# Kernel tuning notes

Hardware: AMD Instinct MI355X
Metric: run time of the kernel (lower is better)

## Reference

```python
import jax, jax.numpy as jnp
import numpy as np

N_WIRES = 4
BATCH, SEQ, EMBED, FFN = 8, 512, 512, 2048


def setup_inputs() -> dict:
    key = jax.random.key(0)
    k_x, k_w1, k_w2 = jax.random.split(key, 3)
    x = jax.random.normal(k_x, (BATCH, SEQ, EMBED), dtype=jnp.float32)
    # Linear params (torch Linear: y = x @ W^T + b; we store pre-transposed)
    W1 = jax.random.normal(k_w1, (EMBED, FFN), dtype=jnp.float32) / np.sqrt(EMBED)
    b1 = jnp.zeros((FFN,), dtype=jnp.float32)
    W2 = jax.random.normal(k_w2, (FFN, EMBED), dtype=jnp.float32) / np.sqrt(FFN)
    b2 = jnp.zeros((EMBED,), dtype=jnp.float32)
    return {"x": x, "W1": W1, "b1": b1, "W2": W2, "b2": b2}


def reference(x, W1, b1, W2, b2):
    b, s, d = x.shape
    flat = x.reshape(b * s, d)                      # [n, d], n = b*s
    # Quantum kernel: circuit RY(x_i) then RY(-y_i) per wire on |0..0>;
    # |0..0> amplitude = prod_i cos((x_i - y_i)/2); only first n_wires feats used
    # (reset_states(1) + states.view(-1)[0] selects batch row 0 of the reshape).
    f = flat[:, :N_WIRES]                           # [n, nw]
    half_diff = (f[:, None, :] - f[None, :, :]) * 0.5   # [n, n, nw]
    gram = jnp.abs(jnp.prod(jnp.cos(half_diff), axis=-1))  # [n, n]
    out = gram @ flat                               # [n, d]
    h = jax.nn.relu(out @ W1 + b1)                  # [n, ffn]  (dropout = eval identity)
    y = h @ W2 + b2                                 # [n, d]
    return y.reshape(b, s, d)
```

## Files before the change

kernel.cpp:

```cpp
#include <hip/hip_runtime.h>
#include <hip/hip_bf16.h>
#include <stdint.h>

using bf = __bf16;
typedef __attribute__((ext_vector_type(8))) __bf16 bf16x8;
typedef __attribute__((ext_vector_type(4))) float f32x4;
typedef __attribute__((ext_vector_type(4))) int i32x4;

#define M_TOT 4096
#define D_EMB 512
#define F_FFN 2048

__device__ __forceinline__ void gload_lds16(const void* g, void* l) {
  __builtin_amdgcn_global_load_lds(
      (const __attribute__((address_space(1))) uint32_t*)g,
      (__attribute__((address_space(3))) uint32_t*)l, 16, 0, 0);
}

__device__ __forceinline__ int swz128(int row, int b) {
  return row * 128 + (b ^ ((row & 7) << 4));
}
__device__ __forceinline__ bf16x8 ldf128(const char* base, int row, int b) {
  return *(const bf16x8*)(base + swz128(row, b));
}
__device__ __forceinline__ i32x4 ldf128i(const char* base, int row, int b) {
  return *(const i32x4*)(base + swz128(row, b));
}
template <int CHUNKS>
__device__ __forceinline__ void stage_rows4(const void* gsrc, size_t ld_bytes, char* lbase,
                                            int wave, int lane) {
  const int rsub = lane >> 3, csub = lane & 7;
  const int sc = csub ^ rsub;
#pragma unroll
  for (int i = 0; i < CHUNKS / 4; ++i) {
    int chunk = wave + i * 4;
    int row = chunk * 8 + rsub;
    gload_lds16((const char*)gsrc + (size_t)row * ld_bytes + sc * 16, lbase + chunk * 1024);
  }
}
__device__ __forceinline__ int quant_i8(float x, float s) {
  float v = x * s;
  v = fminf(127.f, fmaxf(-127.f, v));
  return (int)rintf(v);
}

#define NB_SGEN 1024
#define NT_FT   2048
#define NT_W1   1024
#define NT_W2   1024

__global__ __launch_bounds__(256) void k_prep(const float* __restrict__ x,
                                              const float* __restrict__ W1,
                                              const float* __restrict__ W2,
                                              int8_t* __restrict__ fi8, bf* __restrict__ w1T,
                                              bf* __restrict__ w2T, int8_t* __restrict__ S) {
  __shared__ __align__(16) char smem[32768];
  const int bid = blockIdx.x, tid = threadIdx.x;

  if (bid < NB_SGEN) {
    char* phiL = smem;
    char* st = smem + 16384;
    const int e = bid & 7, idx = bid >> 3;
    const int jt = e * 4 + (idx & 3);
    const int mt = idx >> 2;
    const int m0 = mt * 128;
    const int j0 = jt * 128;
    {
      int g = (tid < 128) ? (m0 + tid) : (j0 + tid - 128);
      float c[4], s[4];
#pragma unroll
      for (int k = 0; k < 4; ++k) {
        float f = x[(size_t)g * D_EMB + k] * 0.5f;
        sincosf(f, &s[k], &c[k]);
      }
      bf* row = (bf*)(phiL + tid * 64);
#pragma unroll
      for (int m = 0; m < 16; ++m) {
        float p = 1.0f;
#pragma unroll
        for (int k = 0; k < 4; ++k) p *= ((m >> k) & 1) ? s[k] : c[k];
        row[m] = (bf)p;
      }
#pragma unroll
      for (int m = 16; m < 32; ++m) row[m] = (bf)0.0f;
    }
    __syncthreads();

    const int wave = tid >> 6, lane = tid & 63;
    const int lr = lane & 15, lg = lane >> 4;
    const bf16x8 a0 = *(const bf16x8*)(phiL + (wave * 32 + lr) * 64 + lg * 16);
    const bf16x8 a1 = *(const bf16x8*)(phiL + (wave * 32 + 16 + lr) * 64 + lg * 16);

    const int mb0 = wave * 32 + lg * 4;
    const int key = (lr & 7) << 4;
#pragma unroll
    for (int jf = 0; jf < 8; ++jf) {
      bf16x8 b = *(const bf16x8*)(phiL + (128 + jf * 16 + lr) * 64 + lg * 16);
      f32x4 s0 = __builtin_amdgcn_mfma_f32_16x16x32_bf16(a0, b, f32x4{0.f, 0.f, 0.f, 0.f}, 0, 0, 0);
      f32x4 s1 = __builtin_amdgcn_mfma_f32_16x16x32_bf16(a1, b, f32x4{0.f, 0.f, 0.f, 0.f}, 0, 0, 0);
      uint32_t w0 = 0, w1 = 0;
#pragma unroll
      for (int r = 0; r < 4; ++r) {
        uint32_t q0 = (uint32_t)min(127, (int)rintf(fabsf(s0[r]) * 127.f));
        uint32_t q1 = (uint32_t)min(127, (int)rintf(fabsf(s1[r]) * 127.f));
        w0 |= q0 << (8 * r);
        w1 |= q1 << (8 * r);
      }
      int jrow = jf * 16 + lr;
      *(uint32_t*)(st + jrow * 128 + (mb0 ^ key)) = w0;
      *(uint32_t*)(st + jrow * 128 + ((mb0 + 16) ^ key)) = w1;
    }
    __syncthreads();
#pragma unroll
    for (int i = 0; i < 4; ++i) {
      int idx2 = tid + i * 256;
      int jrow = idx2 >> 3, seg = idx2 & 7;
      i32x4 v = *(const i32x4*)(st + jrow * 128 + ((seg * 16) ^ ((jrow & 7) << 4)));
      *(i32x4*)(S + (size_t)(j0 + jrow) * M_TOT + m0 + seg * 16) = v;
    }
    return;
  }

  float(*tile)[33] = (float(*)[33])smem;
  const int tx = tid & 31, ty = tid >> 5;
  if (bid < NB_SGEN + NT_FT) {
    int b2 = bid - NB_SGEN;
    int c0 = (b2 % (D_EMB / 32)) * 32, r0 = (b2 / (D_EMB / 32)) * 32;
#pragma unroll
    for (int i = 0; i < 32; i += 8)
      tile[ty + i][tx] = x[(size_t)(r0 + ty + i) * D_EMB + c0 + tx];
    __syncthreads();
#pragma unroll
    for (int i = 0; i < 32; i += 8)
      fi8[(size_t)(c0 + ty + i) * M_TOT + r0 + tx] = (int8_t)quant_i8(tile[tx][ty + i], 15.875f);
  } else if (bid < NB_SGEN + NT_FT + NT_W1) {
    int b2 = bid - NB_SGEN - NT_FT;
    int c0 = (b2 % (F_FFN / 32)) * 32, r0 = (b2 / (F_FFN / 32)) * 32;
#pragma unroll
    for (int i = 0; i < 32; i += 8)
      tile[ty + i][tx] = W1[(size_t)(r0 + ty + i) * F_FFN + c0 + tx];
    __syncthreads();
#pragma unroll
    for (int i = 0; i < 32; i += 8)
      w1T[(size_t)(c0 + ty + i) * D_EMB + r0 + tx] = (bf)tile[tx][ty + i];
  } else {
    int b2 = bid - NB_SGEN - NT_FT - NT_W1;
    int c0 = (b2 % (D_EMB / 32)) * 32, r0 = (b2 / (D_EMB / 32)) * 32;
#pragma unroll
    for (int i = 0; i < 32; i += 8)
      tile[ty + i][tx] = W2[(size_t)(r0 + ty + i) * D_EMB + c0 + tx];
    __syncthreads();
#pragma unroll
    for (int i = 0; i < 32; i += 8)
      w2T[(size_t)(c0 + ty + i) * F_FFN + r0 + tx] = (bf)tile[tx][ty + i];
  }
}

template <int OUTMODE>
__global__ __launch_bounds__(256, 3) void k_g64(const bf* __restrict__ A, const bf* __restrict__ BT,
                                                const float* __restrict__ bias, void* __restrict__ out,
                                                int N, int K) {
  constexpr int BUF = 16384;
  __shared__ __align__(16) char sm[3 * BUF];

  const int tid = threadIdx.x;
  const int wave = tid >> 6, lane = tid & 63;
  const int lr = lane & 15, lg = lane >> 4;
  const int wm = wave & 1, wn = wave >> 1;

  const int lin = blockIdx.x;
  const int e = lin & 7, jj = lin >> 3;
  const int bm = e * 8 + (jj & 7), bn = jj >> 3;
  const int m0 = bm * 64, n0 = bn * 64;

  f32x4 acc[2][2];
#pragma unroll
  for (int i = 0; i < 2; ++i)
#pragma unroll
    for (int f = 0; f < 2; ++f) acc[i][f] = f32x4{0.f, 0.f, 0.f, 0.f};

  const size_t ldb = (size_t)K * 2;
  stage_rows4<8>(A + (size_t)m0 * K, ldb, sm, wave, lane);
  stage_rows4<8>(BT + (size_t)n0 * K, ldb, sm + 8192, wave, lane);
  stage_rows4<8>(A + (size_t)m0 * K + 64, ldb, sm + BUF, wave, lane);
  stage_rows4<8>(BT + (size_t)n0 * K + 64, ldb, sm + BUF + 8192, wave, lane);

  const int NT = K / 64;
  for (int t = 0; t < NT; ++t) {
    char* aTc = sm + (t % 3) * BUF;
    char* bTc = aTc + 8192;
    if (t + 1 < NT) asm volatile("s_waitcnt vmcnt(4)" ::: "memory");
    else            asm volatile("s_waitcnt vmcnt(0)" ::: "memory");
    __builtin_amdgcn_s_barrier();

    if (t + 2 < NT) {
      char* aTn = sm + ((t + 2) % 3) * BUF;
      stage_rows4<8>(A + (size_t)m0 * K + (t + 2) * 64, ldb, aTn, wave, lane);
      stage_rows4<8>(BT + (size_t)n0 * K + (t + 2) * 64, ldb, aTn + 8192, wave, lane);
    }
#pragma unroll
    for (int ksl = 0; ksl < 2; ++ksl) {
      bf16x8 a[2], b[2];
#pragma unroll
      for (int i = 0; i < 2; ++i) a[i] = ldf128(aTc, wm * 32 + i * 16 + lr, (ksl * 32 + lg * 8) * 2);
#pragma unroll
      for (int f = 0; f < 2; ++f) b[f] = ldf128(bTc, wn * 32 + f * 16 + lr, (ksl * 32 + lg * 8) * 2);
#pragma unroll
      for (int i = 0; i < 2; ++i)
#pragma unroll
        for (int f = 0; f < 2; ++f)
          acc[i][f] = __builtin_amdgcn_mfma_f32_16x16x32_bf16(a[i], b[f], acc[i][f], 0, 0, 0);
    }
  }

#pragma unroll
  for (int f = 0; f < 2; ++f) {
    int n = n0 + wn * 32 + f * 16 + lr;
    float bv = bias[n];
#pragma unroll
    for (int i = 0; i < 2; ++i)
#pragma unroll
      for (int r = 0; r < 4; ++r) {
        int m = m0 + wm * 32 + i * 16 + lg * 4 + r;
        float v = acc[i][f][r] + bv;
        if (OUTMODE == 1) {
          v = v > 0.f ? v : 0.f;
          ((bf*)out)[(size_t)m * N + n] = (bf)v;
        } else {
          ((float*)out)[(size_t)m * N + n] = v;
        }
      }
  }
}

__global__ __launch_bounds__(256, 3) void k_gi64(const int8_t* __restrict__ S,
                                                 const int8_t* __restrict__ FT,
                                                 bf* __restrict__ outb) {
  constexpr int BUF = 16384;
  __shared__ __align__(16) char sm[3 * BUF];

  const int tid = threadIdx.x;
  const int wave = tid >> 6, lane = tid & 63;
  const int lr = lane & 15, lg = lane >> 4;
  const int wm = wave & 1, wn = wave >> 1;

  const int lin = blockIdx.x;
  const int e = lin & 7, jj = lin >> 3;
  const int bm = e * 8 + (jj & 7), bn = jj >> 3;
  const int m0 = bm * 64, n0 = bn * 64;

  i32x4 acc[2][2];
#pragma unroll
  for (int i = 0; i < 2; ++i)
#pragma unroll
    for (int f = 0; f < 2; ++f) acc[i][f] = i32x4{0, 0, 0, 0};

  stage_rows4<8>(S + (size_t)m0 * M_TOT, M_TOT, sm, wave, lane);
  stage_rows4<8>(FT + (size_t)n0 * M_TOT, M_TOT, sm + 8192, wave, lane);
  stage_rows4<8>(S + (size_t)m0 * M_TOT + 128, M_TOT, sm + BUF, wave, lane);
  stage_rows4<8>(FT + (size_t)n0 * M_TOT + 128, M_TOT, sm + BUF + 8192, wave, lane);

  constexpr int NT = M_TOT / 128;
  for (int t = 0; t < NT; ++t) {
    char* aTc = sm + (t % 3) * BUF;
    char* bTc = aTc + 8192;
    if (t + 1 < NT) asm volatile("s_waitcnt vmcnt(4)" ::: "memory");
    else            asm volatile("s_waitcnt vmcnt(0)" ::: "memory");
    __builtin_amdgcn_s_barrier();

    if (t + 2 < NT) {
      char* aTn = sm + ((t + 2) % 3) * BUF;
      stage_rows4<8>(S + (size_t)m0 * M_TOT + (t + 2) * 128, M_TOT, aTn, wave, lane);
      stage_rows4<8>(FT + (size_t)n0 * M_TOT + (t + 2) * 128, M_TOT, aTn + 8192, wave, lane);
    }
#pragma unroll
    for (int ksub = 0; ksub < 2; ++ksub) {
      i32x4 a[2], b[2];
#pragma unroll
      for (int i = 0; i < 2; ++i) a[i] = ldf128i(aTc, wm * 32 + i * 16 + lr, ksub * 64 + lg * 16);
#pragma unroll
      for (int f = 0; f < 2; ++f) b[f] = ldf128i(bTc, wn * 32 + f * 16 + lr, ksub * 64 + lg * 16);
#pragma unroll
      for (int i = 0; i < 2; ++i)
#pragma unroll
        for (int f = 0; f < 2; ++f)
          acc[i][f] = __builtin_amdgcn_mfma_i32_16x16x64_i8(a[i], b[f], acc[i][f], 0, 0, 0);
    }
  }

  constexpr float SCALE = 8.0f / 16129.0f;
#pragma unroll
  for (int f = 0; f < 2; ++f) {
    int n = n0 + wn * 32 + f * 16 + lr;
#pragma unroll
    for (int i = 0; i < 2; ++i)
#pragma unroll
      for (int r = 0; r < 4; ++r) {
        int m = m0 + wm * 32 + i * 16 + lg * 4 + r;
        outb[(size_t)m * D_EMB + n] = (bf)((float)acc[i][f][r] * SCALE);
      }
  }
}

constexpr size_t OFF_FI8  = 0;
constexpr size_t OFF_OUTB = OFF_FI8 + (size_t)D_EMB * M_TOT;
constexpr size_t OFF_W1T  = OFF_OUTB + (size_t)M_TOT * D_EMB * 2;
constexpr size_t OFF_W2T  = OFF_W1T + (size_t)F_FFN * D_EMB * 2;
constexpr size_t OFF_S    = OFF_W2T + (size_t)D_EMB * F_FFN * 2;
constexpr size_t OFF_HB   = OFF_S;

extern "C" void kernel_launch(void* const* d_in, const int* in_sizes, int n_in,
                              void* d_out, int out_size, void* d_ws, size_t ws_size,
                              hipStream_t stream) {
  const float* x  = (const float*)d_in[0];
  const float* W1 = (const float*)d_in[1];
  const float* b1 = (const float*)d_in[2];
  const float* W2 = (const float*)d_in[3];
  const float* b2 = (const float*)d_in[4];
  float* y = (float*)d_out;
  char* ws = (char*)d_ws;

  int8_t* fi8 = (int8_t*)(ws + OFF_FI8);
  bf* outb    = (bf*)(ws + OFF_OUTB);
  bf* w1T     = (bf*)(ws + OFF_W1T);
  bf* w2T     = (bf*)(ws + OFF_W2T);
  int8_t* S   = (int8_t*)(ws + OFF_S);
  bf* hb      = (bf*)(ws + OFF_HB);

  k_prep<<<dim3(NB_SGEN + NT_FT + NT_W1 + NT_W2), 256, 0, stream>>>(x, W1, W2, fi8, w1T, w2T, S);

  k_gi64<<<dim3(512), 256, 0, stream>>>(S, fi8, outb);

  k_g64<1><<<dim3(2048), 256, 0, stream>>>(outb, w1T, b1, (void*)hb, F_FFN, D_EMB);
  k_g64<0><<<dim3(512), 256, 0, stream>>>(hb, w2T, b2, (void*)y, D_EMB, F_FFN);
}
```

Baseline: 64.85 us.

## Deepen GEMM LDS pipeline to four stages and vectorize feature load

Both the bf16 GEMM kernel and the int8 gram GEMM kernel move from a 3-buffer to a 4-buffer LDS ring. They prefetch three k-tiles ahead with adjusted vmcnt waits, aiming to hide more global-load latency. This raises LDS per block to 64 KB and lowers the launch-bounds occupancy hint from 3 to 2 blocks, so fewer blocks may be resident per CU. The prep kernel also loads its four x features with a single 16-byte vector read instead of four scalar reads.

```diff
diff --git a/kernel.cpp b/kernel.cpp
--- a/kernel.cpp
+++ b/kernel.cpp
@@ -67,12 +67,10 @@
     const int j0 = jt * 128;
     {
       int g = (tid < 128) ? (m0 + tid) : (j0 + tid - 128);
+      f32x4 xv = *(const f32x4*)(x + (size_t)g * D_EMB);
       float c[4], s[4];
 #pragma unroll
-      for (int k = 0; k < 4; ++k) {
-        float f = x[(size_t)g * D_EMB + k] * 0.5f;
-        sincosf(f, &s[k], &c[k]);
-      }
+      for (int k = 0; k < 4; ++k) sincosf(xv[k] * 0.5f, &s[k], &c[k]);
       bf* row = (bf*)(phiL + tid * 64);
 #pragma unroll
       for (int m = 0; m < 16; ++m) {
@@ -157,11 +155,11 @@
 }
 
 template <int OUTMODE>
-__global__ __launch_bounds__(256, 3) void k_g64(const bf* __restrict__ A, const bf* __restrict__ BT,
+__global__ __launch_bounds__(256, 2) void k_g64(const bf* __restrict__ A, const bf* __restrict__ BT,
                                                 const float* __restrict__ bias, void* __restrict__ out,
                                                 int N, int K) {
   constexpr int BUF = 16384;
-  __shared__ __align__(16) char sm[3 * BUF];
+  __shared__ __align__(16) char sm[4 * BUF];
 
   const int tid = threadIdx.x;
   const int wave = tid >> 6, lane = tid & 63;
@@ -180,23 +178,25 @@
     for (int f = 0; f < 2; ++f) acc[i][f] = f32x4{0.f, 0.f, 0.f, 0.f};
 
   const size_t ldb = (size_t)K * 2;
-  stage_rows4<8>(A + (size_t)m0 * K, ldb, sm, wave, lane);
-  stage_rows4<8>(BT + (size_t)n0 * K, ldb, sm + 8192, wave, lane);
-  stage_rows4<8>(A + (size_t)m0 * K + 64, ldb, sm + BUF, wave, lane);
-  stage_rows4<8>(BT + (size_t)n0 * K + 64, ldb, sm + BUF + 8192, wave, lane);
-
   const int NT = K / 64;
+#pragma unroll
+  for (int p = 0; p < 3; ++p) {
+    stage_rows4<8>(A + (size_t)m0 * K + p * 64, ldb, sm + p * BUF, wave, lane);
+    stage_rows4<8>(BT + (size_t)n0 * K + p * 64, ldb, sm + p * BUF + 8192, wave, lane);
+  }
+
   for (int t = 0; t < NT; ++t) {
-    char* aTc = sm + (t % 3) * BUF;
+    char* aTc = sm + (t & 3) * BUF;
     char* bTc = aTc + 8192;
-    if (t + 1 < NT) asm volatile("s_waitcnt vmcnt(4)" ::: "memory");
-    else            asm volatile("s_waitcnt vmcnt(0)" ::: "memory");
+    if (t + 2 < NT)      asm volatile("s_waitcnt vmcnt(8)" ::: "memory");
+    else if (t + 1 < NT) asm volatile("s_waitcnt vmcnt(4)" ::: "memory");
+    else                 asm volatile("s_waitcnt vmcnt(0)" ::: "memory");
     __builtin_amdgcn_s_barrier();
 
-    if (t + 2 < NT) {
-      char* aTn = sm + ((t + 2) % 3) * BUF;
-      stage_rows4<8>(A + (size_t)m0 * K + (t + 2) * 64, ldb, aTn, wave, lane);
-      stage_rows4<8>(BT + (size_t)n0 * K + (t + 2) * 64, ldb, aTn + 8192, wave, lane);
+    if (t + 3 < NT) {
+      char* aTn = sm + ((t + 3) & 3) * BUF;
+      stage_rows4<8>(A + (size_t)m0 * K + (t + 3) * 64, ldb, aTn, wave, lane);
+      stage_rows4<8>(BT + (size_t)n0 * K + (t + 3) * 64, ldb, aTn + 8192, wave, lane);
     }
 #pragma unroll
     for (int ksl = 0; ksl < 2; ++ksl) {
@@ -233,11 +233,11 @@
   }
 }
 
-__global__ __launch_bounds__(256, 3) void k_gi64(const int8_t* __restrict__ S,
+__global__ __launch_bounds__(256, 2) void k_gi64(const int8_t* __restrict__ S,
                                                  const int8_t* __restrict__ FT,
                                                  bf* __restrict__ outb) {
   constexpr int BUF = 16384;
-  __shared__ __align__(16) char sm[3 * BUF];
+  __shared__ __align__(16) char sm[4 * BUF];
 
   const int tid = threadIdx.x;
   const int wave = tid >> 6, lane = tid & 63;
@@ -255,23 +255,25 @@
 #pragma unroll
     for (int f = 0; f < 2; ++f) acc[i][f] = i32x4{0, 0, 0, 0};
 
-  stage_rows4<8>(S + (size_t)m0 * M_TOT, M_TOT, sm, wave, lane);
-  stage_rows4<8>(FT + (size_t)n0 * M_TOT, M_TOT, sm + 8192, wave, lane);
-  stage_rows4<8>(S + (size_t)m0 * M_TOT + 128, M_TOT, sm + BUF, wave, lane);
-  stage_rows4<8>(FT + (size_t)n0 * M_TOT + 128, M_TOT, sm + BUF + 8192, wave, lane);
-
   constexpr int NT = M_TOT / 128;
+#pragma unroll
+  for (int p = 0; p < 3; ++p) {
+    stage_rows4<8>(S + (size_t)m0 * M_TOT + p * 128, M_TOT, sm + p * BUF, wave, lane);
+    stage_rows4<8>(FT + (size_t)n0 * M_TOT + p * 128, M_TOT, sm + p * BUF + 8192, wave, lane);
+  }
+
   for (int t = 0; t < NT; ++t) {
-    char* aTc = sm + (t % 3) * BUF;
+    char* aTc = sm + (t & 3) * BUF;
     char* bTc = aTc + 8192;
-    if (t + 1 < NT) asm volatile("s_waitcnt vmcnt(4)" ::: "memory");
-    else            asm volatile("s_waitcnt vmcnt(0)" ::: "memory");
+    if (t + 2 < NT)      asm volatile("s_waitcnt vmcnt(8)" ::: "memory");
+    else if (t + 1 < NT) asm volatile("s_waitcnt vmcnt(4)" ::: "memory");
+    else                 asm volatile("s_waitcnt vmcnt(0)" ::: "memory");
     __builtin_amdgcn_s_barrier();
 
-    if (t + 2 < NT) {
-      char* aTn = sm + ((t + 2) % 3) * BUF;
-      stage_rows4<8>(S + (size_t)m0 * M_TOT + (t + 2) * 128, M_TOT, aTn, wave, lane);
-      stage_rows4<8>(FT + (size_t)n0 * M_TOT + (t + 2) * 128, M_TOT, aTn + 8192, wave, lane);
+    if (t + 3 < NT) {
+      char* aTn = sm + ((t + 3) & 3) * BUF;
+      stage_rows4<8>(S + (size_t)m0 * M_TOT + (t + 3) * 128, M_TOT, aTn, wave, lane);
+      stage_rows4<8>(FT + (size_t)n0 * M_TOT + (t + 3) * 128, M_TOT, aTn + 8192, wave, lane);
     }
 #pragma unroll
     for (int ksub = 0; ksub < 2; ++ksub) {
```

Result: slower. 66.67 us (+2.8%).
